# Kernel tuning notes

Measured on AMD Instinct MI355X. Metric: run time of the kernel, lower is better.

## Reference

```python
import jax, jax.numpy as jnp
import numpy as np

N = 8192
IN_F = 64
OUT_F = 64
D_INT = 32
ALPHA = 0.2  # LeakyReLU negative slope


def setup_inputs() -> dict:
    key = jax.random.key(0)
    k1, k2, k3, k4 = jax.random.split(key, 4)
    x = jax.random.normal(k1, (N, IN_F), dtype=jnp.float32)
    adj = jnp.ones((N, N), dtype=bool)  # unused by the original forward math
    intent_embeds = jax.random.normal(k2, (N, D_INT), dtype=jnp.float32)
    # Xavier-uniform-like init scales (gain 1.414)
    limW = 1.414 * np.sqrt(6.0 / (IN_F + OUT_F))
    W = jax.random.uniform(k3, (IN_F, OUT_F), dtype=jnp.float32, minval=-limW, maxval=limW)
    a_len = 2 * OUT_F + 2 * D_INT
    lima = 1.414 * np.sqrt(6.0 / (a_len + 1))
    a = jax.random.uniform(k4, (a_len, 1), dtype=jnp.float32, minval=-lima, maxval=lima)
    return {"input": x, "adj": adj, "intent_embeds": intent_embeds, "W": W, "a": a}


def reference(input, adj, intent_embeds, W, a):
    # h: [N, F]
    h = input @ W
    F_ = h.shape[1]
    a = a[:, 0]
    a_src, a_dst = a[:F_], a[F_:2 * F_]
    b_src, b_dst = a[2 * F_:2 * F_ + D_INT], a[2 * F_ + D_INT:]
    # Additive score decomposes exactly: e[i,j] = lrelu(s_i + t_j)
    s = h @ a_src + intent_embeds @ b_src          # [N]
    t = h @ a_dst + intent_embeds @ b_dst          # [N]
    e = jax.nn.leaky_relu(s[:, None] + t[None, :], negative_slope=ALPHA)  # [N, N]
    # NOTE: original applies softmax over dim=0 (source axis), no adj masking
    attention = jax.nn.softmax(e, axis=0)
    h_prime = attention @ h                        # [N, F]
    return jax.nn.elu(h_prime)
```

## Files before the change

kernel.cpp:

```cpp
#include <hip/hip_runtime.h>
#include <cstdint>
#include <cstddef>

#define N_NODES 8192
#define F_OUT   64
#define DINT    32
#define ALPHA   0.2f

__global__ __launch_bounds__(64) void k_h_st(
    const float* __restrict__ x, const float* __restrict__ ie,
    const float* __restrict__ W, const float* __restrict__ a,
    float* __restrict__ h, float* __restrict__ s, float* __restrict__ t)
{
    const int i = blockIdx.x;
    const int f = threadIdx.x;
    const float* xr = x + (size_t)i * 64;

    float acc = 0.f;
    #pragma unroll 16
    for (int k = 0; k < 64; ++k)
        acc = fmaf(xr[k], W[k * 64 + f], acc);

    h[(size_t)i * 64 + f] = acc;

    float ps = acc * a[f];
    float pt = acc * a[64 + f];
    if (f < DINT) {
        float e = ie[(size_t)i * DINT + f];
        ps = fmaf(e, a[128 + f], ps);
        pt = fmaf(e, a[160 + f], pt);
    }
    #pragma unroll
    for (int m = 1; m < 64; m <<= 1) {
        ps += __shfl_xor(ps, m, 64);
        pt += __shfl_xor(pt, m, 64);
    }
    if (f == 0) { s[i] = ps; t[i] = pt; }
}

__global__ __launch_bounds__(256) void k_ranks(
    const float* __restrict__ s, const float* __restrict__ t,
    float* __restrict__ smax,
    int* __restrict__ pos, int* __restrict__ inv_t,
    float* __restrict__ t_sorted, int* __restrict__ q_sorted,
    float* __restrict__ se1, float* __restrict__ se2)
{
    __shared__ __align__(16) unsigned long long u_sh[2048];
    __shared__ __align__(16) float f_sh[2048];
    const int wave = threadIdx.x >> 6, lane = threadIdx.x & 63;
    const int which = blockIdx.y;
    const int key0 = blockIdx.x * 32 + wave * 8;

    const float* __restrict__ karr = (which == 0) ? s : t;
    const float* __restrict__ oarr = (which == 0) ? t : s;

    float kf[8], nk[8];
    unsigned long long ku[8];
    #pragma unroll
    for (int l = 0; l < 8; ++l) {
        kf[l] = karr[key0 + l];
        unsigned int b = __float_as_uint(kf[l]);
        b = (b & 0x80000000u) ? ~b : (b | 0x80000000u);
        ku[l] = ((unsigned long long)b << 32) | (unsigned int)(key0 + l);
        nk[l] = -kf[l];
    }

    int c1[8] = {0,0,0,0,0,0,0,0}, c2[8] = {0,0,0,0,0,0,0,0};
    unsigned long long mx = 0ull;

    for (int c = 0; c < 4; ++c) {
        const int base = c * 2048;
        {
            const int e0 = threadIdx.x * 8;
            float4 a0 = *reinterpret_cast<const float4*>(&karr[base + e0]);
            float4 a1 = *reinterpret_cast<const float4*>(&karr[base + e0 + 4]);
            float4 b0 = *reinterpret_cast<const float4*>(&oarr[base + e0]);
            float4 b1 = *reinterpret_cast<const float4*>(&oarr[base + e0 + 4]);
            const float av[8] = {a0.x,a0.y,a0.z,a0.w,a1.x,a1.y,a1.z,a1.w};
            #pragma unroll
            for (int e = 0; e < 8; ++e) {
                unsigned int b = __float_as_uint(av[e]);
                b = (b & 0x80000000u) ? ~b : (b | 0x80000000u);
                u_sh[e0 + e] = ((unsigned long long)b << 32)
                             | (unsigned int)(base + e0 + e);
            }
            *reinterpret_cast<float4*>(&f_sh[e0])     = b0;
            *reinterpret_cast<float4*>(&f_sh[e0 + 4]) = b1;
        }
        __syncthreads();

        for (int k = lane * 4; k < 2048; k += 256) {
            const ulonglong2 p0 = *reinterpret_cast<const ulonglong2*>(&u_sh[k]);
            const ulonglong2 p1 = *reinterpret_cast<const ulonglong2*>(&u_sh[k + 2]);
            const float4 fv = *reinterpret_cast<const float4*>(&f_sh[k]);
            if (which == 0) {
                unsigned long long m01 = p0.x > p0.y ? p0.x : p0.y;
                unsigned long long m23 = p1.x > p1.y ? p1.x : p1.y;
                unsigned long long m03 = m01 > m23 ? m01 : m23;
                mx = mx > m03 ? mx : m03;
            }
            #pragma unroll
            for (int l = 0; l < 8; ++l) {
                c1[l] += (int)(p0.x < ku[l]) + (int)(p0.y < ku[l])
                       + (int)(p1.x < ku[l]) + (int)(p1.y < ku[l]);
                c2[l] += (int)(fv.x < nk[l]) + (int)(fv.y < nk[l])
                       + (int)(fv.z < nk[l]) + (int)(fv.w < nk[l]);
            }
        }
        __syncthreads();
    }

    int pk[8];
    #pragma unroll
    for (int l = 0; l < 8; ++l) pk[l] = c1[l] * 16384 + c2[l];
    #pragma unroll
    for (int m = 1; m < 64; m <<= 1) {
        #pragma unroll
        for (int l = 0; l < 8; ++l) pk[l] += __shfl_xor(pk[l], m, 64);
    }

    if (which == 0) {
        #pragma unroll
        for (int m = 1; m < 64; m <<= 1) {
            unsigned long long o = __shfl_xor(mx, m, 64);
            mx = mx > o ? mx : o;
        }
        if (lane == 0) {
            unsigned int b = (unsigned int)(mx >> 32);
            b = (b & 0x80000000u) ? (b ^ 0x80000000u) : ~b;
            const float smax_f = __uint_as_float(b);
            if (key0 == 0) smax[0] = smax_f;
            #pragma unroll
            for (int l = 0; l < 8; ++l) {
                const int idx = key0 + l;
                const int r1 = pk[l] >> 14, r2 = pk[l] & 16383;
                pos[idx] = r2;
                const float d = kf[l] - smax_f;
                se1[r1] = __expf(d);
                se2[r1] = __expf(ALPHA * d);
            }
        }
    } else if (lane == 0) {
        #pragma unroll
        for (int l = 0; l < 8; ++l) {
            const int idx = key0 + l;
            const int r1 = pk[l] >> 14, r2 = pk[l] & 16383;
            inv_t[r1] = idx;
            t_sorted[r1] = kf[l];
            q_sorted[r1] = r2;
        }
    }
}

__global__ __launch_bounds__(1024) void k_mid(
    const float* __restrict__ se1, const float* __restrict__ se2,
    const float* __restrict__ smax_p,
    const float* __restrict__ t_sorted, const int* __restrict__ q_sorted,
    float* __restrict__ cf1, float* __restrict__ cf2)
{
    __shared__ float suf1[8200];
    __shared__ float pre2[8200];
    __shared__ double wred[2][16];
    const int tid = threadIdx.x, wave = tid >> 6, lane = tid & 63;
    const int base = tid * 8;

    double l1[8], l2[8], s1 = 0.0, s2 = 0.0;
    #pragma unroll
    for (int k = 0; k < 8; ++k) {
        l1[k] = (double)se1[base + k]; s1 += l1[k];
        l2[k] = (double)se2[base + k]; s2 += l2[k];
    }
    double i1 = s1, i2 = s2;
    #pragma unroll
    for (int off = 1; off < 64; off <<= 1) {
        double v1 = __shfl_up(i1, off, 64);
        double v2 = __shfl_up(i2, off, 64);
        if (lane >= off) { i1 += v1; i2 += v2; }
    }
    if (lane == 63) { wred[0][wave] = i1; wred[1][wave] = i2; }
    __syncthreads();
    double off1 = 0, off2 = 0, tot1 = 0, tot2 = 0;
    #pragma unroll
    for (int w = 0; w < 16; ++w) {
        const double a = wred[0][w], b = wred[1][w];
        if (w < wave) { off1 += a; off2 += b; }
        tot1 += a; tot2 += b;
    }
    double run1 = off1 + (i1 - s1);
    double run2 = off2 + (i2 - s2);
    #pragma unroll
    for (int k = 0; k < 8; ++k) {
        suf1[base + k] = (float)(tot1 - run1); run1 += l1[k];
        pre2[base + k] = (float)run2;          run2 += l2[k];
    }
    if (tid == 1023) { suf1[8192] = 0.f; pre2[8192] = (float)tot2; }
    __syncthreads();

    const float smax = smax_p[0];
    #pragma unroll
    for (int k = 0; k < 8; ++k) {
        const int r = tid + k * 1024;
        const float tj = t_sorted[r];
        const float zc = smax + tj;
        const float c = fmaxf(zc, ALPHA * zc);
        const float E1 = __expf(zc - c);
        const float E2 = __expf(ALPHA * zc - c);
        const int qj = q_sorted[r];
        const float D = E1 * suf1[qj] + E2 * pre2[qj];
        const float invD = 1.f / D;
        cf1[r] = E1 * invD;
        cf2[r] = E2 * invD;
    }
}

__global__ __launch_bounds__(256) void k_tilesum(
    const float* __restrict__ h, const int* __restrict__ inv_t,
    const float* __restrict__ cf1, const float* __restrict__ cf2,
    float* __restrict__ T1, float* __restrict__ T2)
{
    const int tile = blockIdx.x;
    const int wave = threadIdx.x >> 6, f = threadIdx.x & 63;
    const int r0 = tile * 128 + wave * 32;
    float a1 = 0.f, a2 = 0.f;
    for (int k = 0; k < 32; ++k) {
        const int r = r0 + k;
        const int j = inv_t[r];
        const float v = h[(size_t)j * 64 + f];
        a1 = fmaf(cf1[r], v, a1);
        a2 = fmaf(cf2[r], v, a2);
    }
    __shared__ float red[2][4][64];
    red[0][wave][f] = a1; red[1][wave][f] = a2;
    __syncthreads();
    if (wave == 0)
        T1[tile * 64 + f] = red[0][0][f] + red[0][1][f] + red[0][2][f] + red[0][3][f];
    else if (wave == 1)
        T2[tile * 64 + f] = red[1][0][f] + red[1][1][f] + red[1][2][f] + red[1][3][f];
}

__global__ __launch_bounds__(64) void k_scan2(
    const float* __restrict__ h, const int* __restrict__ inv_t,
    const float* __restrict__ cf1, const float* __restrict__ cf2,
    const float* __restrict__ T1, const float* __restrict__ T2,
    float* __restrict__ S1, float* __restrict__ S2)
{
    const int tile = blockIdx.x, arr = blockIdx.y, f = threadIdx.x;
    if (arr == 0) {
        float acc = 0.f;
        for (int tt = tile + 1; tt < 64; ++tt) acc += T1[tt * 64 + f];
        if (tile == 63) S1[(size_t)8192 * 64 + f] = 0.f;
        for (int rb = 15; rb >= 0; --rb) {
            const int r0 = tile * 128 + rb * 8;
            float v[8];
            #pragma unroll
            for (int k = 0; k < 8; ++k)
                v[k] = cf1[r0 + k] * h[(size_t)inv_t[r0 + k] * 64 + f];
            #pragma unroll
            for (int k = 7; k >= 0; --k) { acc += v[k]; S1[(size_t)(r0 + k) * 64 + f] = acc; }
        }
    } else {
        float acc = 0.f;
        for (int tt = 0; tt < tile; ++tt) acc += T2[tt * 64 + f];
        for (int rb = 0; rb < 16; ++rb) {
            const int r0 = tile * 128 + rb * 8;
            float v[8];
            #pragma unroll
            for (int k = 0; k < 8; ++k)
                v[k] = cf2[r0 + k] * h[(size_t)inv_t[r0 + k] * 64 + f];
            #pragma unroll
            for (int k = 0; k < 8; ++k) { S2[(size_t)(r0 + k) * 64 + f] = acc; acc += v[k]; }
        }
        if (tile == 63) S2[(size_t)8192 * 64 + f] = acc;
    }
}

__global__ __launch_bounds__(256) void k_out(
    const float* __restrict__ s, const float* __restrict__ smax_p,
    const int* __restrict__ pos,
    const float* __restrict__ S1, const float* __restrict__ S2,
    float* __restrict__ out)
{
    const int i = blockIdx.x * 4 + (threadIdx.x >> 6);
    const int f = threadIdx.x & 63;
    const float d = s[i] - smax_p[0];
    const float e1 = __expf(d), e2 = __expf(ALPHA * d);
    const int p = pos[i];
    const float v = fmaf(e1, S1[(size_t)p * 64 + f], e2 * S2[(size_t)p * 64 + f]);
    out[(size_t)i * 64 + f] = v > 0.f ? v : expm1f(v);
}

extern "C" void kernel_launch(void* const* d_in, const int* in_sizes, int n_in,
                              void* d_out, int out_size, void* d_ws, size_t ws_size,
                              hipStream_t stream)
{
    const float* x  = (const float*)d_in[0];
    const float* ie = (const float*)d_in[2];
    const float* W  = (const float*)d_in[3];
    const float* a  = (const float*)d_in[4];
    float* out = (float*)d_out;

    float* p = (float*)d_ws;
    float* h        = p; p += (size_t)N_NODES * F_OUT;
    float* s        = p; p += N_NODES;
    float* t        = p; p += N_NODES;
    float* smax     = p; p += 16;
    float* se1      = p; p += N_NODES;
    float* se2      = p; p += N_NODES;
    float* t_sorted = p; p += N_NODES;
    float* cf1      = p; p += N_NODES;
    float* cf2      = p; p += N_NODES;
    float* T1       = p; p += 64 * 64;
    float* T2       = p; p += 64 * 64;
    float* S1       = p; p += (size_t)(N_NODES + 1) * F_OUT + 64;
    float* S2       = p; p += (size_t)(N_NODES + 1) * F_OUT + 64;
    int* pos        = (int*)p; p += N_NODES;
    int* inv_t      = (int*)p; p += N_NODES;
    int* q_sorted   = (int*)p; p += N_NODES;

    k_h_st    <<<N_NODES, 64, 0, stream>>>(x, ie, W, a, h, s, t);
    k_ranks   <<<dim3(N_NODES / 32, 2), 256, 0, stream>>>(s, t, smax,
                      pos, inv_t, t_sorted, q_sorted, se1, se2);
    k_mid     <<<1, 1024, 0, stream>>>(se1, se2, smax, t_sorted, q_sorted,
                      cf1, cf2);
    k_tilesum <<<64, 256, 0, stream>>>(h, inv_t, cf1, cf2, T1, T2);
    k_scan2   <<<dim3(64, 2), 64, 0, stream>>>(h, inv_t, cf1, cf2, T1, T2, S1, S2);
    k_out     <<<N_NODES / 4, 256, 0, stream>>>(s, smax, pos, S1, S2, out);
}
```

Baseline: 364.1 us.

## Fuse tile-sum and scan into one cooperative kernel, precompute packed sort keys

Merges the tile-sum and two-pass scan kernels into a single cooperative kernel that keeps the gathered h rows in registers across a grid-wide sync, so the second gather of h and one kernel launch go away. The packed 64-bit sort keys are now built once in the first kernel and loaded directly by the rank kernel, instead of every block rebuilding them from the floats. This relies on cooperative launch and a grid barrier across 64 blocks, and the rank kernel now reads 8-byte keys from global memory where it used to read floats.

```diff
diff --git a/kernel.cpp b/kernel.cpp
--- a/kernel.cpp
+++ b/kernel.cpp
@@ -1,4 +1,5 @@
 #include <hip/hip_runtime.h>
+#include <hip/hip_cooperative_groups.h>
 #include <cstdint>
 #include <cstddef>
 
@@ -7,10 +8,19 @@
 #define DINT    32
 #define ALPHA   0.2f
 
+namespace cg = cooperative_groups;
+
+__device__ __forceinline__ unsigned long long pack_vi(float v, int idx) {
+    unsigned int b = __float_as_uint(v);
+    b = (b & 0x80000000u) ? ~b : (b | 0x80000000u);
+    return ((unsigned long long)b << 32) | (unsigned int)idx;
+}
+
 __global__ __launch_bounds__(64) void k_h_st(
     const float* __restrict__ x, const float* __restrict__ ie,
     const float* __restrict__ W, const float* __restrict__ a,
-    float* __restrict__ h, float* __restrict__ s, float* __restrict__ t)
+    float* __restrict__ h, float* __restrict__ s, float* __restrict__ t,
+    unsigned long long* __restrict__ su, unsigned long long* __restrict__ tu)
 {
     const int i = blockIdx.x;
     const int f = threadIdx.x;
@@ -35,11 +45,17 @@
         ps += __shfl_xor(ps, m, 64);
         pt += __shfl_xor(pt, m, 64);
     }
-    if (f == 0) { s[i] = ps; t[i] = pt; }
+    if (f == 0) {
+        s[i] = ps; t[i] = pt;
+        su[i] = pack_vi(ps, i);
+        tu[i] = pack_vi(pt, i);
+    }
 }
 
 __global__ __launch_bounds__(256) void k_ranks(
     const float* __restrict__ s, const float* __restrict__ t,
+    const unsigned long long* __restrict__ su,
+    const unsigned long long* __restrict__ tu,
     float* __restrict__ smax,
     int* __restrict__ pos, int* __restrict__ inv_t,
     float* __restrict__ t_sorted, int* __restrict__ q_sorted,
@@ -47,11 +63,14 @@
 {
     __shared__ __align__(16) unsigned long long u_sh[2048];
     __shared__ __align__(16) float f_sh[2048];
-    const int wave = threadIdx.x >> 6, lane = threadIdx.x & 63;
+    const int tid  = threadIdx.x;
+    const int wave = __builtin_amdgcn_readfirstlane(tid) >> 6;
+    const int lane = tid & 63;
     const int which = blockIdx.y;
     const int key0 = blockIdx.x * 32 + wave * 8;
 
     const float* __restrict__ karr = (which == 0) ? s : t;
+    const unsigned long long* __restrict__ kuarr = (which == 0) ? su : tu;
     const float* __restrict__ oarr = (which == 0) ? t : s;
 
     float kf[8], nk[8];
@@ -59,9 +78,7 @@
     #pragma unroll
     for (int l = 0; l < 8; ++l) {
         kf[l] = karr[key0 + l];
-        unsigned int b = __float_as_uint(kf[l]);
-        b = (b & 0x80000000u) ? ~b : (b | 0x80000000u);
-        ku[l] = ((unsigned long long)b << 32) | (unsigned int)(key0 + l);
+        ku[l] = kuarr[key0 + l];
         nk[l] = -kf[l];
     }
 
@@ -70,22 +87,10 @@
 
     for (int c = 0; c < 4; ++c) {
         const int base = c * 2048;
-        {
-            const int e0 = threadIdx.x * 8;
-            float4 a0 = *reinterpret_cast<const float4*>(&karr[base + e0]);
-            float4 a1 = *reinterpret_cast<const float4*>(&karr[base + e0 + 4]);
-            float4 b0 = *reinterpret_cast<const float4*>(&oarr[base + e0]);
-            float4 b1 = *reinterpret_cast<const float4*>(&oarr[base + e0 + 4]);
-            const float av[8] = {a0.x,a0.y,a0.z,a0.w,a1.x,a1.y,a1.z,a1.w};
-            #pragma unroll
-            for (int e = 0; e < 8; ++e) {
-                unsigned int b = __float_as_uint(av[e]);
-                b = (b & 0x80000000u) ? ~b : (b | 0x80000000u);
-                u_sh[e0 + e] = ((unsigned long long)b << 32)
-                             | (unsigned int)(base + e0 + e);
-            }
-            *reinterpret_cast<float4*>(&f_sh[e0])     = b0;
-            *reinterpret_cast<float4*>(&f_sh[e0 + 4]) = b1;
+        #pragma unroll
+        for (int e = 0; e < 8; ++e) {
+            u_sh[tid + e * 256] = kuarr[base + tid + e * 256];
+            f_sh[tid + e * 256] = oarr[base + tid + e * 256];
         }
         __syncthreads();
 
@@ -213,64 +218,77 @@
     }
 }
 
-__global__ __launch_bounds__(256) void k_tilesum(
+__global__ __launch_bounds__(256) void k_scan(
     const float* __restrict__ h, const int* __restrict__ inv_t,
     const float* __restrict__ cf1, const float* __restrict__ cf2,
-    float* __restrict__ T1, float* __restrict__ T2)
+    float* __restrict__ T1, float* __restrict__ T2,
+    float* __restrict__ S1, float* __restrict__ S2)
 {
     const int tile = blockIdx.x;
-    const int wave = threadIdx.x >> 6, f = threadIdx.x & 63;
-    const int r0 = tile * 128 + wave * 32;
-    float a1 = 0.f, a2 = 0.f;
+    const int wave = __builtin_amdgcn_readfirstlane(threadIdx.x) >> 6;
+    const int f = threadIdx.x & 63;
+    const int rbase = tile * 128 + wave * 32;
+
+    float hv[32];
+    #pragma unroll
+    for (int k = 0; k < 32; ++k)
+        hv[k] = h[(size_t)inv_t[rbase + k] * 64 + f];
+
+    float w1 = 0.f, w2 = 0.f;
+    #pragma unroll
     for (int k = 0; k < 32; ++k) {
-        const int r = r0 + k;
-        const int j = inv_t[r];
-        const float v = h[(size_t)j * 64 + f];
-        a1 = fmaf(cf1[r], v, a1);
-        a2 = fmaf(cf2[r], v, a2);
-    }
-    __shared__ float red[2][4][64];
-    red[0][wave][f] = a1; red[1][wave][f] = a2;
+        w1 = fmaf(cf1[rbase + k], hv[k], w1);
+        w2 = fmaf(cf2[rbase + k], hv[k], w2);
+    }
+    __shared__ float ws[2][4][64];
+    ws[0][wave][f] = w1;
+    ws[1][wave][f] = w2;
     __syncthreads();
     if (wave == 0)
-        T1[tile * 64 + f] = red[0][0][f] + red[0][1][f] + red[0][2][f] + red[0][3][f];
+        T1[tile * 64 + f] = ws[0][0][f] + ws[0][1][f] + ws[0][2][f] + ws[0][3][f];
     else if (wave == 1)
-        T2[tile * 64 + f] = red[1][0][f] + red[1][1][f] + red[1][2][f] + red[1][3][f];
-}
-
-__global__ __launch_bounds__(64) void k_scan2(
-    const float* __restrict__ h, const int* __restrict__ inv_t,
-    const float* __restrict__ cf1, const float* __restrict__ cf2,
-    const float* __restrict__ T1, const float* __restrict__ T2,
-    float* __restrict__ S1, float* __restrict__ S2)
-{
-    const int tile = blockIdx.x, arr = blockIdx.y, f = threadIdx.x;
-    if (arr == 0) {
-        float acc = 0.f;
-        for (int tt = tile + 1; tt < 64; ++tt) acc += T1[tt * 64 + f];
-        if (tile == 63) S1[(size_t)8192 * 64 + f] = 0.f;
-        for (int rb = 15; rb >= 0; --rb) {
-            const int r0 = tile * 128 + rb * 8;
-            float v[8];
-            #pragma unroll
-            for (int k = 0; k < 8; ++k)
-                v[k] = cf1[r0 + k] * h[(size_t)inv_t[r0 + k] * 64 + f];
-            #pragma unroll
-            for (int k = 7; k >= 0; --k) { acc += v[k]; S1[(size_t)(r0 + k) * 64 + f] = acc; }
-        }
-    } else {
-        float acc = 0.f;
-        for (int tt = 0; tt < tile; ++tt) acc += T2[tt * 64 + f];
-        for (int rb = 0; rb < 16; ++rb) {
-            const int r0 = tile * 128 + rb * 8;
-            float v[8];
-            #pragma unroll
-            for (int k = 0; k < 8; ++k)
-                v[k] = cf2[r0 + k] * h[(size_t)inv_t[r0 + k] * 64 + f];
-            #pragma unroll
-            for (int k = 0; k < 8; ++k) { S2[(size_t)(r0 + k) * 64 + f] = acc; acc += v[k]; }
-        }
-        if (tile == 63) S2[(size_t)8192 * 64 + f] = acc;
+        T2[tile * 64 + f] = ws[1][0][f] + ws[1][1][f] + ws[1][2][f] + ws[1][3][f];
+
+    __threadfence();
+    cg::this_grid().sync();
+
+    {
+        float a0 = 0.f, a1 = 0.f, a2 = 0.f, a3 = 0.f;
+        int tt = tile + 1;
+        for (; tt + 3 < 64; tt += 4) {
+            a0 += T1[(tt + 0) * 64 + f];
+            a1 += T1[(tt + 1) * 64 + f];
+            a2 += T1[(tt + 2) * 64 + f];
+            a3 += T1[(tt + 3) * 64 + f];
+        }
+        for (; tt < 64; ++tt) a0 += T1[tt * 64 + f];
+        float acc = (a0 + a1) + (a2 + a3);
+        for (int w = wave + 1; w < 4; ++w) acc += ws[0][w][f];
+        #pragma unroll
+        for (int k = 31; k >= 0; --k) {
+            acc = fmaf(cf1[rbase + k], hv[k], acc);
+            S1[(size_t)(rbase + k) * 64 + f] = acc;
+        }
+        if (tile == 63 && wave == 0) S1[(size_t)8192 * 64 + f] = 0.f;
+    }
+    {
+        float a0 = 0.f, a1 = 0.f, a2 = 0.f, a3 = 0.f;
+        int tt = 0;
+        for (; tt + 3 < tile; tt += 4) {
+            a0 += T2[(tt + 0) * 64 + f];
+            a1 += T2[(tt + 1) * 64 + f];
+            a2 += T2[(tt + 2) * 64 + f];
+            a3 += T2[(tt + 3) * 64 + f];
+        }
+        for (; tt < tile; ++tt) a0 += T2[tt * 64 + f];
+        float acc = (a0 + a1) + (a2 + a3);
+        for (int w = 0; w < wave; ++w) acc += ws[1][w][f];
+        #pragma unroll
+        for (int k = 0; k < 32; ++k) {
+            S2[(size_t)(rbase + k) * 64 + f] = acc;
+            acc = fmaf(cf2[rbase + k], hv[k], acc);
+        }
+        if (tile == 63 && wave == 3) S2[(size_t)8192 * 64 + f] = acc;
     }
 }
 
@@ -280,7 +298,7 @@
     const float* __restrict__ S1, const float* __restrict__ S2,
     float* __restrict__ out)
 {
-    const int i = blockIdx.x * 4 + (threadIdx.x >> 6);
+    const int i = blockIdx.x * 4 + (__builtin_amdgcn_readfirstlane(threadIdx.x) >> 6);
     const int f = threadIdx.x & 63;
     const float d = s[i] - smax_p[0];
     const float e1 = __expf(d), e2 = __expf(ALPHA * d);
@@ -316,13 +334,18 @@
     int* pos        = (int*)p; p += N_NODES;
     int* inv_t      = (int*)p; p += N_NODES;
     int* q_sorted   = (int*)p; p += N_NODES;
-
-    k_h_st    <<<N_NODES, 64, 0, stream>>>(x, ie, W, a, h, s, t);
-    k_ranks   <<<dim3(N_NODES / 32, 2), 256, 0, stream>>>(s, t, smax,
-                      pos, inv_t, t_sorted, q_sorted, se1, se2);
-    k_mid     <<<1, 1024, 0, stream>>>(se1, se2, smax, t_sorted, q_sorted,
-                      cf1, cf2);
-    k_tilesum <<<64, 256, 0, stream>>>(h, inv_t, cf1, cf2, T1, T2);
-    k_scan2   <<<dim3(64, 2), 64, 0, stream>>>(h, inv_t, cf1, cf2, T1, T2, S1, S2);
-    k_out     <<<N_NODES / 4, 256, 0, stream>>>(s, smax, pos, S1, S2, out);
-}
+    unsigned long long* su = (unsigned long long*)p; p += 2 * N_NODES;
+    unsigned long long* tu = (unsigned long long*)p; p += 2 * N_NODES;
+
+    k_h_st <<<N_NODES, 64, 0, stream>>>(x, ie, W, a, h, s, t, su, tu);
+    k_ranks<<<dim3(N_NODES / 32, 2), 256, 0, stream>>>(s, t, su, tu, smax,
+                    pos, inv_t, t_sorted, q_sorted, se1, se2);
+    k_mid  <<<1, 1024, 0, stream>>>(se1, se2, smax, t_sorted, q_sorted, cf1, cf2);
+    {
+        void* kargs[8] = { (void*)&h, (void*)&inv_t, (void*)&cf1, (void*)&cf2,
+                           (void*)&T1, (void*)&T2, (void*)&S1, (void*)&S2 };
+        (void)hipLaunchCooperativeKernel((const void*)k_scan, dim3(64), dim3(256),
+                                         kargs, 0u, stream);
+    }
+    k_out  <<<N_NODES / 4, 256, 0, stream>>>(s, smax, pos, S1, S2, out);
+}
```

New measurement: 391.1 us. +7.4%, slower.
